# Kernel tuning notes

Hardware: AMD Instinct MI355X
Metric: run time of the kernel (lower is better)

The kernel has to match this reference:

```python
import jax, jax.numpy as jnp
import numpy as np

HID, STEM, BN_OUT, STEM_OUT, MLP = 256, 64, 128, 64, 128
BN_WS, STEM_WS = 5, 17
N, H_BN, W_BN, H_VIS, W_VIS = 4096, 128, 128, 1024, 1024


def setup_inputs() -> dict:
    key = jax.random.key(0)
    ks = jax.random.split(key, 24)
    f32 = jnp.float32
    def rn(k, shape, s=0.05):
        return jax.random.normal(k, shape, f32) * s
    return dict(
        bottleneck=rn(ks[0], (1, HID, H_BN, W_BN), 1.0),
        vis_stem_features=rn(ks[1], (1, STEM, H_VIS, W_VIS), 1.0),
        source_positions_vis=jax.random.uniform(ks[2], (N, 2), f32, 10.0, W_VIS - 10.0),
        pixel_to_sky=rn(ks[3], (N, 2, 2), 0.1),
        fused_h=H_BN, fused_w=W_BN, vis_h=H_VIS, vis_w=W_VIS,
        dw_w=rn(ks[4], (HID, 1, 7, 7)), dw_b=rn(ks[5], (HID,)),
        ln_g=jnp.ones((HID,), f32), ln_b=jnp.zeros((HID,), f32),
        pw1_w=rn(ks[6], (4 * HID, HID)), pw1_b=rn(ks[7], (4 * HID,)),
        pw2_w=rn(ks[8], (HID, 4 * HID)), pw2_b=rn(ks[9], (HID,)),
        cn_gamma=jnp.full((HID,), 1e-2, f32),
        bn1x1_w=rn(ks[10], (BN_OUT, HID, 1, 1)), bn1x1_b=rn(ks[11], (BN_OUT,)),
        st1_w=rn(ks[12], (STEM_OUT, STEM, 3, 3)), st1_b=rn(ks[13], (STEM_OUT,)),
        st2_w=rn(ks[14], (STEM_OUT, STEM_OUT, 3, 3)), st2_b=rn(ks[15], (STEM_OUT,)),
        h1_w=rn(ks[16], (MLP, BN_OUT + STEM_OUT)), h1_b=rn(ks[17], (MLP,)),
        h2_w=rn(ks[18], (MLP, MLP)), h2_b=rn(ks[19], (MLP,)),
        h3_w=rn(ks[20], (3, MLP)),
        h3_b=jnp.array([0.0, 0.0, float(np.log(0.05))], f32),
    )


def _gelu(x):
    return jax.nn.gelu(x, approximate=False)


def _conv2d(x, w, b, padding, groups=1):
    y = jax.lax.conv_general_dilated(
        x, w, (1, 1), [(padding, padding), (padding, padding)],
        dimension_numbers=('NCHW', 'OIHW', 'NCHW'), feature_group_count=groups)
    return y + b[None, :, None, None]


def _bilinear_windows(fm, pos, ws):
    """fm [1,C,H,W], pos [N,2] pixel coords -> [N,C,ws,ws].
    Matches torch grid_sample(mode=bilinear, padding=zeros, align_corners=True)
    with the module's normalize/unnormalize, i.e. direct pixel-coord sampling."""
    C, H, W = fm.shape[1:]
    fm2 = fm[0]
    half = ws // 2
    off = jnp.arange(-half, half + 1, dtype=pos.dtype)
    gy, gx = jnp.meshgrid(off, off, indexing='ij')
    xs = gx[None] + pos[:, 0, None, None]   # [N,ws,ws]
    ys = gy[None] + pos[:, 1, None, None]
    x0 = jnp.floor(xs); y0 = jnp.floor(ys)
    wx1 = xs - x0; wy1 = ys - y0
    x0i = x0.astype(jnp.int32); y0i = y0.astype(jnp.int32)
    def gather(yi, xi, w):
        valid = (yi >= 0) & (yi < H) & (xi >= 0) & (xi < W)
        v = fm2[:, jnp.clip(yi, 0, H - 1), jnp.clip(xi, 0, W - 1)]  # [C,N,ws,ws]
        return v * (w * valid)[None]
    out = (gather(y0i, x0i, (1 - wy1) * (1 - wx1))
           + gather(y0i, x0i + 1, (1 - wy1) * wx1)
           + gather(y0i + 1, x0i, wy1 * (1 - wx1))
           + gather(y0i + 1, x0i + 1, wy1 * wx1))
    return jnp.transpose(out, (1, 0, 2, 3))


def _gauss(ws):
    t = jnp.linspace(-1.0, 1.0, ws)
    yy, xx = jnp.meshgrid(t, t, indexing='ij')
    g = jnp.exp(-(xx ** 2 + yy ** 2) / (2 * 0.4 ** 2))
    return g / g.sum()


def _convnext(x, dw_w, dw_b, ln_g, ln_b, pw1_w, pw1_b, pw2_w, pw2_b, gamma):
    r = x
    x = _conv2d(x, dw_w, dw_b, padding=3, groups=x.shape[1])  # depthwise 7x7
    mu = x.mean(1, keepdims=True)
    var = ((x - mu) ** 2).mean(1, keepdims=True)
    x = (x - mu) / jnp.sqrt(var + 1e-6)
    x = x * ln_g[None, :, None, None] + ln_b[None, :, None, None]
    x = jnp.einsum('nchw,oc->nohw', x, pw1_w) + pw1_b[None, :, None, None]
    x = _gelu(x)
    x = jnp.einsum('nchw,oc->nohw', x, pw2_w) + pw2_b[None, :, None, None]
    return r + gamma[None, :, None, None] * x


def _forward(bottleneck, vis_stem_features, source_positions_vis, pixel_to_sky,
             dw_w, dw_b, ln_g, ln_b, pw1_w, pw1_b, pw2_w, pw2_b, cn_gamma,
             bn1x1_w, bn1x1_b, st1_w, st1_b, st2_w, st2_b,
             h1_w, h1_b, h2_w, h2_b, h3_w, h3_b,
             fused_h, fused_w, vis_h, vis_w):
    scale = jnp.array([fused_w / vis_w, fused_h / vis_h], source_positions_vis.dtype)
    pos_bn = source_positions_vis * scale
    # bottleneck branch: 5x5 windows -> ConvNeXt -> 1x1 conv -> GELU -> gauss pool
    bn_win = _bilinear_windows(bottleneck, pos_bn, BN_WS)              # [N,256,5,5]
    bn_feat = _convnext(bn_win, dw_w, dw_b, ln_g, ln_b, pw1_w, pw1_b, pw2_w, pw2_b, cn_gamma)
    bn_feat = _gelu(_conv2d(bn_feat, bn1x1_w, bn1x1_b, padding=0))     # [N,128,5,5]
    bn_vec = (bn_feat * _gauss(BN_WS)[None, None]).sum((-2, -1))       # [N,128]
    st_win = _bilinear_windows(vis_stem_features, source_positions_vis, STEM_WS)
    st = _gelu(_conv2d(st_win, st1_w, st1_b, padding=1))
    st = _gelu(_conv2d(st, st2_w, st2_b, padding=1))                   # [N,64,17,17]
    st_vec = (st * _gauss(STEM_WS)[None, None]).sum((-2, -1))          # [N,64]
    # head MLP
    x = jnp.concatenate([bn_vec, st_vec], axis=1)                      # [N,192]
    x = _gelu(x @ h1_w.T + h1_b)
    x = _gelu(x @ h2_w.T + h2_b)
    out = x @ h3_w.T + h3_b                                            # [N,3]
    dx_px, dy_px = out[:, 0], out[:, 1]
    log_sigma = jnp.clip(out[:, 2], -6.0, 3.0)
    pix = jnp.stack([dx_px, dy_px], axis=1)                            # [N,2]
    pred_sky = jnp.einsum('nij,nj->ni', pixel_to_sky, pix)             # [N,2]
    confidence = 1.0 / jnp.maximum(jnp.exp(log_sigma), 1e-4)
    return pred_sky, dx_px, dy_px, log_sigma, confidence


def reference(bottleneck, vis_stem_features, source_positions_vis, pixel_to_sky,
              fused_h, fused_w, vis_h, vis_w,
              dw_w, dw_b, ln_g, ln_b, pw1_w, pw1_b, pw2_w, pw2_b, cn_gamma,
              bn1x1_w, bn1x1_b, st1_w, st1_b, st2_w, st2_b,
              h1_w, h1_b, h2_w, h2_b, h3_w, h3_b):
    return _forward(bottleneck, vis_stem_features, source_positions_vis, pixel_to_sky,
                    dw_w, dw_b, ln_g, ln_b, pw1_w, pw1_b, pw2_w, pw2_b, cn_gamma,
                    bn1x1_w, bn1x1_b, st1_w, st1_b, st2_w, st2_b,
                    h1_w, h1_b, h2_w, h2_b, h3_w, h3_b,
                    fused_h, fused_w, vis_h, vis_w)
```

## Files before the change

kernel.cpp:

```cpp
#include <hip/hip_runtime.h>
#include <hip/hip_bf16.h>

#define XSTR 28

typedef short short8 __attribute__((ext_vector_type(8)));
typedef float f32x4  __attribute__((ext_vector_type(4)));
typedef float f32x16 __attribute__((ext_vector_type(16)));

__device__ __forceinline__ float gelu_f(float x){
    return 0.5f*x*(1.0f + erff(x*0.70710678118654752f));
}
__device__ __forceinline__ float gelu_q(float x){
    const float z = 1.5957691216057308f*x*(1.0f + 0.044715f*x*x);
    return x / (1.0f + __expf(-z));
}
__device__ __forceinline__ unsigned short f2bf(float f){
    unsigned int u = __float_as_uint(f);
    u += 0x7fffu + ((u>>16)&1u);
    return (unsigned short)(u>>16);
}
__device__ __forceinline__ unsigned int pack2(float a, float b){
    return (unsigned int)f2bf(a) | ((unsigned int)f2bf(b)<<16);
}
__device__ __forceinline__ float bf_lo(unsigned int u){ return __uint_as_float(u<<16); }
__device__ __forceinline__ float bf_hi(unsigned int u){ return __uint_as_float(u & 0xffff0000u); }
__device__ __forceinline__ float bfu(unsigned short v){ return __uint_as_float(((unsigned int)v)<<16); }

__device__ __forceinline__ void fma_row25(const float* __restrict__ row, float w, float* __restrict__ acc){
    const float4* r4 = (const float4*)row;
    float4 a0=r4[0], a1=r4[1], a2=r4[2], a3=r4[3], a4=r4[4], a5=r4[5];
    float a6 = row[24];
    acc[0]+=a0.x*w;  acc[1]+=a0.y*w;  acc[2]+=a0.z*w;  acc[3]+=a0.w*w;
    acc[4]+=a1.x*w;  acc[5]+=a1.y*w;  acc[6]+=a1.z*w;  acc[7]+=a1.w*w;
    acc[8]+=a2.x*w;  acc[9]+=a2.y*w;  acc[10]+=a2.z*w; acc[11]+=a2.w*w;
    acc[12]+=a3.x*w; acc[13]+=a3.y*w; acc[14]+=a3.z*w; acc[15]+=a3.w*w;
    acc[16]+=a4.x*w; acc[17]+=a4.y*w; acc[18]+=a4.z*w; acc[19]+=a4.w*w;
    acc[20]+=a5.x*w; acc[21]+=a5.y*w; acc[22]+=a5.z*w; acc[23]+=a5.w*w;
    acc[24]+=a6*w;
}

__global__ __launch_bounds__(512,4) void bn_branch_mfma(
    const float* __restrict__ bottleneck, const float* __restrict__ pos,
    const float* __restrict__ dw_w, const float* __restrict__ dw_b,
    const float* __restrict__ ln_g, const float* __restrict__ ln_b,
    const float* __restrict__ pw1_b, const float* __restrict__ pw2_b,
    const float* __restrict__ cn_gamma, const float* __restrict__ bn1x1_b,
    const short8* __restrict__ P1v, const short8* __restrict__ P2v,
    const short8* __restrict__ Pbv,
    float* __restrict__ vec_out)
{
    __shared__ __align__(16) unsigned char Xb[64*512];
    __shared__ __align__(16) unsigned char Hc[64*256];
    __shared__ float redA[400], redB[400], muS[56], rsS[56];

    const int n0 = blockIdx.x*2, t = threadIdx.x;
    const int lane = t & 63, w = t >> 6;
    const int mcol = lane & 15, h4 = lane >> 4;
    const int sP = t >> 8, cP = t & 255;

    unsigned int wvp[13];
    float xdw[25];
    {
        const int n = n0 + sP;
        const float px = pos[2*n]*0.125f, py = pos[2*n+1]*0.125f;
        const float fpx = floorf(px), fpy = floorf(py);
        const int ix0 = (int)fpx - 2, iy0 = (int)fpy - 2;
        const float fx = px - fpx, fy = py - fpy;
        const float w00=(1.f-fy)*(1.f-fx), w01=(1.f-fy)*fx, w10=fy*(1.f-fx), w11=fy*fx;
        float wv[25];
        {
            const float* fm = bottleneck + cP*16384;
            float P[6][6];
            #pragma unroll
            for (int r=0;r<6;r++){
                const int y = iy0+r;
                const bool yok = (y>=0)&&(y<128);
                const int yc = y<0?0:(y>127?127:y);
                #pragma unroll
                for (int s=0;s<6;s++){
                    const int x = ix0+s;
                    const bool ok = yok && (x>=0) && (x<128);
                    const int xc = x<0?0:(x>127?127:x);
                    P[r][s] = ok ? fm[yc*128+xc] : 0.f;
                }
            }
            #pragma unroll
            for (int a=0;a<5;a++)
            #pragma unroll
            for (int b=0;b<5;b++)
                wv[a*5+b] = w00*P[a][b]+w01*P[a][b+1]+w10*P[a+1][b]+w11*P[a+1][b+1];
        }
        #pragma unroll
        for (int i=0;i<12;i++) wvp[i] = pack2(wv[2*i], wv[2*i+1]);
        wvp[12] = pack2(wv[24], 0.f);
        {
            float wcr[49];
            const float* wc = dw_w + cP*49;
            #pragma unroll
            for (int k=0;k<49;k++) wcr[k]=wc[k];
            const float bb = dw_b[cP];
            #pragma unroll
            for (int i=0;i<5;i++){
                #pragma unroll
                for (int j=0;j<5;j++){
                    float a = bb;
                    #pragma unroll
                    for (int u=0;u<7;u++){
                        const int y = i+u-3;
                        if (y<0||y>4) continue;
                        #pragma unroll
                        for (int v=0;v<7;v++){
                            const int x = j+v-3;
                            if (x<0||x>4) continue;
                            a += wv[y*5+x]*wcr[u*7+v];
                        }
                    }
                    xdw[i*5+j] = a;
                }
            }
        }
        #pragma unroll
        for (int p=0;p<25;p++){
            const int row = sP*32 + p;
            *(unsigned short*)(Xb + row*512 + ((2*cP) ^ ((row&7)<<4))) = f2bf(xdw[p]);
        }
    }
    __syncthreads();
    if (t < 400){
        const int sp = t>>3, part = t&7;
        const int row = (sp/25)*32 + (sp - (sp/25)*25);
        float a=0.f, b=0.f;
        for (int c=part; c<256; c+=8){
            const float v = bfu(*(const unsigned short*)(Xb + row*512 + ((2*c) ^ ((row&7)<<4))));
            a += v; b += v*v;
        }
        redA[t]=a; redB[t]=b;
    }
    __syncthreads();
    if (t < 50){
        float a=0.f, b=0.f;
        #pragma unroll
        for (int s=0;s<8;s++){ a+=redA[t*8+s]; b+=redB[t*8+s]; }
        const float m = a*(1.f/256.f);
        const float var = b*(1.f/256.f) - m*m;
        muS[t]=m; rsS[t]=rsqrtf(var+1e-6f);
    }
    __syncthreads();
    {
        const float g = ln_g[cP], bb = ln_b[cP];
        #pragma unroll
        for (int p=0;p<25;p++){
            const int row = sP*32 + p;
            const float v = (xdw[p]-muS[sP*25+p])*rsS[sP*25+p]*g + bb;
            *(unsigned short*)(Xb + row*512 + ((2*cP) ^ ((row&7)<<4))) = f2bf(v);
        }
    }
    __syncthreads();

    f32x4 acc2[2][4];
    #pragma unroll
    for (int ml=0;ml<2;ml++)
        #pragma unroll
        for (int nt=0;nt<4;nt++) acc2[ml][nt]=0.f;

    for (int ch=0; ch<8; ++ch){
        const int mt = ch*8 + w;
        f32x4 a1[4];
        #pragma unroll
        for (int nt=0;nt<4;nt++) a1[nt]=0.f;
        #pragma unroll
        for (int kk=0; kk<8; ++kk){
            const short8 av = P1v[((mt<<3)+kk)*64 + lane];
            #pragma unroll
            for (int nt=0; nt<4; ++nt){
                const int row = nt*16 + mcol;
                const int ad = row*512 + ((kk*64 + h4*16) ^ ((row&7)<<4));
                const short8 bv = *(const short8*)(Xb + ad);
                a1[nt] = __builtin_amdgcn_mfma_f32_16x16x32_bf16(av, bv, a1[nt], 0,0,0);
            }
        }
        {
            const float4 b1v = *(const float4*)(pw1_b + mt*16 + h4*4);
            #pragma unroll
            for (int nt=0; nt<4; ++nt){
                const int row = nt*16 + mcol;
                const float g0 = gelu_q(a1[nt].x + b1v.x);
                const float g1 = gelu_q(a1[nt].y + b1v.y);
                const float g2 = gelu_q(a1[nt].z + b1v.z);
                const float g3 = gelu_q(a1[nt].w + b1v.w);
                const int ad = row*256 + ((w*32 + h4*8) ^ ((row&7)<<4));
                *(uint2*)(Hc + ad) = make_uint2(pack2(g0,g1), pack2(g2,g3));
            }
        }
        __syncthreads();
        #pragma unroll
        for (int ml=0; ml<2; ++ml){
            const int mtc = w*2 + ml;
            #pragma unroll
            for (int kk2=0; kk2<4; ++kk2){
                const short8 av = P2v[(mtc*32 + (ch*4 + kk2))*64 + lane];
                #pragma unroll
                for (int nt=0; nt<4; ++nt){
                    const int row = nt*16 + mcol;
                    const int ad = row*256 + ((kk2*64 + h4*16) ^ ((row&7)<<4));
                    const short8 bv = *(const short8*)(Hc + ad);
                    acc2[ml][nt] = __builtin_amdgcn_mfma_f32_16x16x32_bf16(av, bv, acc2[ml][nt], 0,0,0);
                }
            }
        }
        __syncthreads();
    }

    #pragma unroll
    for (int ml=0; ml<2; ++ml){
        const int c0 = (w*2+ml)*16 + h4*4;
        const float4 gm = *(const float4*)(cn_gamma + c0);
        const float4 b2 = *(const float4*)(pw2_b + c0);
        #pragma unroll
        for (int nt=0; nt<4; ++nt){
            const int row = nt*16 + mcol;
            const int ad = row*512 + ((2*c0) ^ ((row&7)<<4));
            const float f0 = gm.x*(acc2[ml][nt].x + b2.x);
            const float f1 = gm.y*(acc2[ml][nt].y + b2.y);
            const float f2 = gm.z*(acc2[ml][nt].z + b2.z);
            const float f3 = gm.w*(acc2[ml][nt].w + b2.w);
            *(uint2*)(Xb + ad) = make_uint2(pack2(f0,f1), pack2(f2,f3));
        }
    }
    __syncthreads();
    #pragma unroll
    for (int p=0;p<25;p++){
        const int row = sP*32 + p;
        unsigned short* ptr = (unsigned short*)(Xb + row*512 + ((2*cP) ^ ((row&7)<<4)));
        const float r = (p&1) ? bf_hi(wvp[p>>1]) : bf_lo(wvp[p>>1]);
        *ptr = f2bf(bfu(*ptr) + r);
    }
    __syncthreads();

    {
        f32x4 a3[4];
        #pragma unroll
        for (int nt=0;nt<4;nt++) a3[nt]=0.f;
        #pragma unroll
        for (int kk=0; kk<8; ++kk){
            const short8 av = Pbv[((w<<3)+kk)*64 + lane];
            #pragma unroll
            for (int nt=0; nt<4; ++nt){
                const int row = nt*16 + mcol;
                const int ad = row*512 + ((kk*64 + h4*16) ^ ((row&7)<<4));
                const short8 bv = *(const short8*)(Xb + ad);
                a3[nt] = __builtin_amdgcn_mfma_f32_16x16x32_bf16(av, bv, a3[nt], 0,0,0);
            }
        }
        const float4 bb = *(const float4*)(bn1x1_b + w*16 + h4*4);
        float e5[5];
        #pragma unroll
        for (int a=0;a<5;a++){
            const float ta = -1.f + 0.5f*a;
            e5[a] = expf(-3.125f*ta*ta);
        }
        const float Sv = e5[0]+e5[1]+e5[2]+e5[3]+e5[4];
        const float invS = 1.0f/(Sv*Sv);
        float sA[2][4];
        #pragma unroll
        for (int s=0;s<2;s++)
            #pragma unroll
            for (int j=0;j<4;j++) sA[s][j]=0.f;
        #pragma unroll
        for (int nt=0; nt<4; ++nt){
            const int row = nt*16 + mcol;
            const int s = row>>5, p = row&31;
            if (p < 25){
                const int pa = p/5, pb = p - pa*5;
                const float g = e5[pa]*e5[pb];
                sA[s][0] += g*gelu_q(a3[nt].x + bb.x);
                sA[s][1] += g*gelu_q(a3[nt].y + bb.y);
                sA[s][2] += g*gelu_q(a3[nt].z + bb.z);
                sA[s][3] += g*gelu_q(a3[nt].w + bb.w);
            }
        }
        #pragma unroll
        for (int off=1; off<16; off<<=1){
            #pragma unroll
            for (int s=0;s<2;s++)
                #pragma unroll
                for (int j=0;j<4;j++) sA[s][j] += __shfl_xor(sA[s][j], off);
        }
        if (mcol == 0){
            const int o = w*16 + h4*4;
            #pragma unroll
            for (int s=0;s<2;s++){
                float* vo = vec_out + (n0+s)*192 + o;
                vo[0]=sA[s][0]*invS; vo[1]=sA[s][1]*invS;
                vo[2]=sA[s][2]*invS; vo[3]=sA[s][3]*invS;
            }
        }
    }
}

__global__ __launch_bounds__(256) void prepack_bn_kernel(
    const float* __restrict__ W1, const float* __restrict__ W2, const float* __restrict__ Wb,
    unsigned short* __restrict__ P1, unsigned short* __restrict__ P2, unsigned short* __restrict__ Pb)
{
    const int tid = blockIdx.x*256 + threadIdx.x;
    const float* src; unsigned short* dst; int row, col, stride, idx;
    if (tid < 32768){
        idx = tid;
        const int frag = idx>>6, l = idx&63;
        row = (frag>>3)*16 + (l&15); col = (frag&7)*32 + (l>>4)*8; stride = 256;
        src = W1; dst = P1;
    } else if (tid < 65536){
        idx = tid - 32768;
        const int frag = idx>>6, l = idx&63;
        row = (frag>>5)*16 + (l&15); col = (frag&31)*32 + (l>>4)*8; stride = 1024;
        src = W2; dst = P2;
    } else if (tid < 69632){
        idx = tid - 65536;
        const int frag = idx>>6, l = idx&63;
        row = (frag>>3)*16 + (l&15); col = (frag&7)*32 + (l>>4)*8; stride = 256;
        src = Wb; dst = Pb;
    } else return;
    const float* s = src + row*stride + col;
    unsigned int v[4];
    #pragma unroll
    for (int j=0;j<4;j++) v[j] = pack2(s[2*j], s[2*j+1]);
    *(uint4*)(dst + (size_t)idx*8) = make_uint4(v[0],v[1],v[2],v[3]);
}

__global__ __launch_bounds__(256,2) void bn_branch_valu(
    const float* __restrict__ bottleneck, const float* __restrict__ pos,
    const float* __restrict__ dw_w, const float* __restrict__ dw_b,
    const float* __restrict__ ln_g, const float* __restrict__ ln_b,
    const float* __restrict__ pw1_w, const float* __restrict__ pw1_b,
    const float* __restrict__ pw2_w, const float* __restrict__ pw2_b,
    const float* __restrict__ cn_gamma,
    const float* __restrict__ bn1x1_w, const float* __restrict__ bn1x1_b,
    float* __restrict__ vec_out)
{
    __shared__ float xln[256*XSTR];
    __shared__ float hbuf[256*XSTR];
    __shared__ float redA[200], redB[200];
    __shared__ float mu[25], rs[25];

    const int n = blockIdx.x;
    const int t = threadIdx.x;
    const int c = t;

    const float px = pos[2*n]*0.125f, py = pos[2*n+1]*0.125f;
    const float fpx = floorf(px), fpy = floorf(py);
    const int ix0 = (int)fpx - 2, iy0 = (int)fpy - 2;
    const float fx = px - fpx, fy = py - fpy;
    const float w00=(1.f-fy)*(1.f-fx), w01=(1.f-fy)*fx, w10=fy*(1.f-fx), w11=fy*fx;

    float wv[25];
    {
        const float* fm = bottleneck + c*16384;
        float P[6][6];
        #pragma unroll
        for (int r=0;r<6;r++){
            const int y = iy0+r;
            const bool yok = (y>=0)&&(y<128);
            const int yc = y<0?0:(y>127?127:y);
            #pragma unroll
            for (int s=0;s<6;s++){
                const int x = ix0+s;
                const bool ok = yok && (x>=0) && (x<128);
                const int xc = x<0?0:(x>127?127:x);
                P[r][s] = ok ? fm[yc*128+xc] : 0.f;
            }
        }
        #pragma unroll
        for (int a=0;a<5;a++)
        #pragma unroll
        for (int b=0;b<5;b++)
            wv[a*5+b] = w00*P[a][b]+w01*P[a][b+1]+w10*P[a+1][b]+w11*P[a+1][b+1];
    }
    {
        float wcr[49];
        const float* wc = dw_w + c*49;
        #pragma unroll
        for (int k=0;k<49;k++) wcr[k]=wc[k];
        const float bb = dw_b[c];
        #pragma unroll
        for (int i=0;i<5;i++){
            #pragma unroll
            for (int j=0;j<5;j++){
                float a = bb;
                #pragma unroll
                for (int u=0;u<7;u++){
                    const int y = i+u-3;
                    if (y<0||y>4) continue;
                    #pragma unroll
                    for (int v=0;v<7;v++){
                        const int x = j+v-3;
                        if (x<0||x>4) continue;
                        a += wv[y*5+x]*wcr[u*7+v];
                    }
                }
                xln[c*XSTR + i*5+j] = a;
            }
        }
    }
    __syncthreads();
    if (t < 200){
        const int p = t>>3, s = t&7;
        float a=0.f, b=0.f;
        for (int cc=s; cc<256; cc+=8){
            const float v = xln[cc*XSTR+p];
            a += v; b += v*v;
        }
        redA[t]=a; redB[t]=b;
    }
    __syncthreads();
    if (t < 25){
        float a=0.f, b=0.f;
        #pragma unroll
        for (int s=0;s<8;s++){ a+=redA[t*8+s]; b+=redB[t*8+s]; }
        const float m = a*(1.f/256.f);
        const float var = b*(1.f/256.f) - m*m;
        mu[t]=m; rs[t]=rsqrtf(var+1e-6f);
    }
    __syncthreads();
    {
        const float g = ln_g[c], bb = ln_b[c];
        #pragma unroll
        for (int p=0;p<25;p++)
            xln[c*XSTR+p] = (xln[c*XSTR+p]-mu[p])*rs[p]*g + bb;
    }
    __syncthreads();
    float acc2[25];
    #pragma unroll
    for (int p=0;p<25;p++) acc2[p]=0.f;
    for (int r=0;r<4;r++){
        const int o = r*256 + t;
        float h[25];
        {
            const float b1 = pw1_b[o];
            #pragma unroll
            for (int p=0;p<25;p++) h[p]=b1;
            const float* wr = pw1_w + o*256;
            for (int cc=0;cc<256;cc++)
                fma_row25(xln + cc*XSTR, wr[cc], h);
            #pragma unroll
            for (int p=0;p<25;p++) h[p]=gelu_f(h[p]);
        }
        __syncthreads();
        #pragma unroll
        for (int p=0;p<25;p++) hbuf[t*XSTR+p]=h[p];
        __syncthreads();
        {
            const float* w2 = pw2_w + t*1024 + r*256;
            for (int k=0;k<256;k++)
                fma_row25(hbuf + k*XSTR, w2[k], acc2);
        }
    }
    {
        const float gam = cn_gamma[c], b2 = pw2_b[c];
        #pragma unroll
        for (int p=0;p<25;p++)
            xln[c*XSTR+p] = wv[p] + gam*(acc2[p]+b2);
    }
    __syncthreads();
    if (t < 128){
        float acc[25];
        #pragma unroll
        for (int p=0;p<25;p++) acc[p]=0.f;
        const float* wr = bn1x1_w + t*256;
        for (int cc=0;cc<256;cc++)
            fma_row25(xln + cc*XSTR, wr[cc], acc);
        const float b = bn1x1_b[t];
        float e5[5];
        #pragma unroll
        for (int a=0;a<5;a++){
            const float ta = -1.f + 0.5f*a;
            e5[a] = expf(-3.125f*ta*ta);
        }
        const float Sv = e5[0]+e5[1]+e5[2]+e5[3]+e5[4];
        float res = 0.f;
        #pragma unroll
        for (int a=0;a<5;a++){
            float rowa = 0.f;
            #pragma unroll
            for (int bb=0;bb<5;bb++)
                rowa += e5[bb]*gelu_f(acc[a*5+bb]+b);
            res += e5[a]*rowa;
        }
        vec_out[n*192+t] = res/(Sv*Sv);
    }
}

__global__ __launch_bounds__(256) void prepack_kernel(
    const float* __restrict__ W1, const float* __restrict__ W2,
    unsigned short* __restrict__ Ap)
{
    const int tid = blockIdx.x*256 + threadIdx.x;
    if (tid >= 9216) return;
    const int conv = tid / 4608;
    const int r = tid - conv*4608;
    const int frag = r >> 6, l = r & 63;
    const int k  = frag >> 3;
    const int kt = (frag >> 1) & 3;
    const int wo = frag & 1;
    const float* W = conv ? W2 : W1;
    const int o  = wo*32 + (l & 31);
    const int c0 = kt*16 + (l >> 5)*8;
    unsigned int v[4];
    #pragma unroll
    for (int jj=0; jj<4; jj++){
        const float f0 = W[o*576 + (c0+2*jj  )*9 + k];
        const float f1 = W[o*576 + (c0+2*jj+1)*9 + k];
        v[jj] = pack2(f0, f1);
    }
    *(uint4*)(Ap + (size_t)tid*8) = make_uint4(v[0], v[1], v[2], v[3]);
}

#define STEM_CONV32(SRC, AP)                                                        \
    _Pragma("unroll")                                                               \
    for (int k=0;k<9;k++){                                                          \
        int tj[3];                                                                  \
        _Pragma("unroll")                                                           \
        for (int j=0;j<3;j++)                                                       \
            tj[j] = (int)sTab[m*90 + (j<cnt ? st+j : st)*9 + k];                    \
        _Pragma("unroll")                                                           \
        for (int kt=0;kt<4;kt++){                                                   \
            const short8 av = (AP)[(k*8 + kt*2 + wo)*64 + lane];                    \
            const int cb = kt*32 + hi16;                                            \
            _Pragma("unroll")                                                       \
            for (int j=0;j<3;j++){                                                  \
                if (j < cnt){                                                       \
                    const short8 bv = *(const short8*)((SRC) + (tj[j] ^ cb));       \
                    acc[j] = __builtin_amdgcn_mfma_f32_32x32x16_bf16(av, bv, acc[j], 0,0,0); \
                }                                                                   \
            }                                                                       \
        }                                                                           \
    }

__global__ __launch_bounds__(512,4) void stem_branch_kernel(
    const float* __restrict__ vis,
    const float* __restrict__ pos,
    const short8* __restrict__ Ap1,
    const float* __restrict__ st1_b,
    const float* __restrict__ st2_b,
    float* __restrict__ vec_out)
{
    __shared__ __align__(16) unsigned char sXt[290*128];
    __shared__ unsigned short sTab[32*90];
    __shared__ float redS[64][4];

    const int n = blockIdx.x;
    const int t = threadIdx.x;
    const int lane = t & 63;
    const int m = lane & 31;
    const int hi = lane >> 5;
    const int hi16 = hi*16;
    const int w = t >> 6;
    const int wo = w & 1;
    const int nh = w >> 1;
    const int st  = nh*3 - (nh==3 ? 1 : 0);
    const int cnt = (nh < 2) ? 3 : 2;

    const float fpx0 = pos[2*n], fpy0 = pos[2*n+1];
    const float fpx = floorf(fpx0), fpy = floorf(fpy0);
    const int ix0 = (int)fpx - 8, iy0 = (int)fpy - 8;
    const float fx = fpx0-fpx, fy = fpy0-fpy;
    const float w00=(1.f-fy)*(1.f-fx), w01=(1.f-fy)*fx, w10=fy*(1.f-fx), w11=fy*fx;

    if (t < 32) *(unsigned int*)(sXt + 289*128 + t*4) = 0u;

    for (int idx = t; idx < 32*90; idx += 512){
        const int mm = idx/90, rem = idx - mm*90;
        const int nt = rem/9, k = rem - nt*9;
        const int p = nt*32 + mm;
        int pp = 289;
        if (p < 289){
            const int py = (p*241)>>12, px = p - py*17;
            const int y = py + k/3 - 1, x = px + (k - (k/3)*3) - 1;
            if (((unsigned)y < 17u) && ((unsigned)x < 17u)) pp = y*17 + x;
        }
        sTab[idx] = (unsigned short)(pp*128 + ((pp&7)<<4));
    }

    for (int task = t; task < 64*17; task += 512){
        const int c  = task & 63;
        const int py = task >> 6;
        const float* r0 = vis + c*1048576 + (iy0+py)*1024 + ix0;
        float a[18], b[18];
        #pragma unroll
        for (int kk=0; kk<18; kk++){ a[kk]=r0[kk]; b[kk]=r0[1024+kk]; }
        #pragma unroll
        for (int px=0; px<17; px++){
            const float v = w00*a[px] + w01*a[px+1] + w10*b[px] + w11*b[px+1];
            const int p = py*17 + px;
            *(unsigned short*)(sXt + p*128 + ((2*c) ^ ((p&7)<<4))) = f2bf(v);
        }
    }
    __syncthreads();

    f32x16 acc[3];
    #pragma unroll
    for (int j=0;j<3;j++) acc[j] = 0.f;
    STEM_CONV32(sXt, Ap1)

    uint2 pk[3][4];
    {
        float4 b4[4];
        #pragma unroll
        for (int rg=0;rg<4;rg++) b4[rg] = *(const float4*)(st1_b + wo*32 + 8*rg + 4*hi);
        #pragma unroll
        for (int j=0;j<3;j++){
            if (j < cnt){
                #pragma unroll
                for (int rg=0;rg<4;rg++){
                    const float v0 = gelu_q(acc[j][4*rg+0] + b4[rg].x);
                    const float v1 = gelu_q(acc[j][4*rg+1] + b4[rg].y);
                    const float v2 = gelu_q(acc[j][4*rg+2] + b4[rg].z);
                    const float v3 = gelu_q(acc[j][4*rg+3] + b4[rg].w);
                    pk[j][rg] = make_uint2(pack2(v0,v1), pack2(v2,v3));
                }
            }
        }
    }
    __syncthreads();

    #pragma unroll
    for (int j=0;j<3;j++){
        if (j < cnt){
            const int p = (st+j)*32 + m;
            if (p < 289){
                const int swz = (p&7)<<4;
                #pragma unroll
                for (int rg=0;rg<4;rg++){
                    const int ch0 = wo*32 + 8*rg + 4*hi;
                    *(uint2*)(sXt + p*128 + ((2*ch0) ^ swz)) = pk[j][rg];
                }
            }
        }
    }
    __syncthreads();

    const short8* Ap2 = Ap1 + 4608;
    #pragma unroll
    for (int j=0;j<3;j++) acc[j] = 0.f;
    STEM_CONV32(sXt, Ap2)

    {
        float4 b4[4];
        #pragma unroll
        for (int rg=0;rg<4;rg++) b4[rg] = *(const float4*)(st2_b + wo*32 + 8*rg + 4*hi);
        float s[16];
        #pragma unroll
        for (int r=0;r<16;r++) s[r]=0.f;
        #pragma unroll
        for (int j=0;j<3;j++){
            if (j < cnt){
                const int p = (st+j)*32 + m;
                if (p < 289){
                    const int py = (p*241)>>12;
                    const int px = p - py*17;
                    const float ty = -1.f + 0.125f*py;
                    const float tx = -1.f + 0.125f*px;
                    const float g = expf(-3.125f*(ty*ty + tx*tx));
                    #pragma unroll
                    for (int rg=0;rg<4;rg++){
                        s[4*rg+0] += g*gelu_q(acc[j][4*rg+0] + b4[rg].x);
                        s[4*rg+1] += g*gelu_q(acc[j][4*rg+1] + b4[rg].y);
                        s[4*rg+2] += g*gelu_q(acc[j][4*rg+2] + b4[rg].z);
                        s[4*rg+3] += g*gelu_q(acc[j][4*rg+3] + b4[rg].w);
                    }
                }
            }
        }
        #pragma unroll
        for (int off=1; off<32; off<<=1){
            #pragma unroll
            for (int r=0;r<16;r++) s[r] += __shfl_xor(s[r], off);
        }
        if (m == 0){
            #pragma unroll
            for (int rg=0;rg<4;rg++)
                #pragma unroll
                for (int e=0;e<4;e++)
                    redS[wo*32 + 8*rg + 4*hi + e][nh] = s[4*rg+e];
        }
    }
    __syncthreads();
    if (t < 64){
        float Sv = 0.f;
        #pragma unroll
        for (int j=0;j<17;j++){
            const float tj = -1.f + 0.125f*j;
            Sv += expf(-3.125f*tj*tj);
        }
        vec_out[n*192+128+t] = (redS[t][0] + redS[t][1] + redS[t][2] + redS[t][3]) / (Sv*Sv);
    }
}

__global__ __launch_bounds__(128) void head16_kernel(
    const float* __restrict__ vec, const float* __restrict__ p2s,
    const float* __restrict__ h1_w, const float* __restrict__ h1_b,
    const float* __restrict__ h2_w, const float* __restrict__ h2_b,
    const float* __restrict__ h3_w, const float* __restrict__ h3_b,
    float* __restrict__ out, int N)
{
    __shared__ float v[16][192];
    __shared__ float x1s[16][132];
    __shared__ float x2s[16][132];
    __shared__ float o3s[16][4];
    const int n0 = blockIdx.x*16, t = threadIdx.x;

    for (int idx=t; idx<16*192; idx+=128){
        const int s = idx/192, k = idx - s*192;
        v[s][k] = vec[n0*192 + idx];
    }
    __syncthreads();
    {
        const int o = t;
        float acc[16];
        const float b = h1_b[o];
        #pragma unroll
        for (int s=0;s<16;s++) acc[s]=b;
        const float4* wr = (const float4*)(h1_w + o*192);
        for (int k4=0;k4<48;k4++){
            const float4 wv4 = wr[k4];
            #pragma unroll
            for (int s=0;s<16;s++){
                const float4 vv = *(const float4*)&v[s][k4*4];
                acc[s] += wv4.x*vv.x + wv4.y*vv.y + wv4.z*vv.z + wv4.w*vv.w;
            }
        }
        #pragma unroll
        for (int s=0;s<16;s++) x1s[s][o] = gelu_f(acc[s]);
    }
    __syncthreads();
    {
        const int o = t;
        float acc[16];
        const float b = h2_b[o];
        #pragma unroll
        for (int s=0;s<16;s++) acc[s]=b;
        const float4* wr = (const float4*)(h2_w + o*128);
        for (int k4=0;k4<32;k4++){
            const float4 wv4 = wr[k4];
            #pragma unroll
            for (int s=0;s<16;s++){
                const float4 vv = *(const float4*)&x1s[s][k4*4];
                acc[s] += wv4.x*vv.x + wv4.y*vv.y + wv4.z*vv.z + wv4.w*vv.w;
            }
        }
        #pragma unroll
        for (int s=0;s<16;s++) x2s[s][o] = gelu_f(acc[s]);
    }
    __syncthreads();
    if (t < 48){
        const int j = t>>4, s = t&15;
        float a = h3_b[j];
        const float* wr = h3_w + j*128;
        for (int k=0;k<128;k++) a += x2s[s][k]*wr[k];
        o3s[s][j] = a;
    }
    __syncthreads();
    if (t < 16){
        const int s = t, n = n0 + s;
        const float dx = o3s[s][0], dy = o3s[s][1];
        float ls = o3s[s][2];
        ls = ls < -6.f ? -6.f : (ls > 3.f ? 3.f : ls);
        const float s0 = p2s[n*4+0]*dx + p2s[n*4+1]*dy;
        const float s1 = p2s[n*4+2]*dx + p2s[n*4+3]*dy;
        const float conf = 1.0f/fmaxf(expf(ls), 1e-4f);
        out[2*n]   = s0;
        out[2*n+1] = s1;
        out[2*N+n] = dx;
        out[3*N+n] = dy;
        out[4*N+n] = ls;
        out[5*N+n] = conf;
    }
}

extern "C" void kernel_launch(void* const* d_in, const int* in_sizes, int n_in,
                              void* d_out, int out_size, void* d_ws, size_t ws_size,
                              hipStream_t stream)
{
    (void)n_in; (void)out_size;
    const float* bottleneck = (const float*)d_in[0];
    const float* vis        = (const float*)d_in[1];
    const float* pos        = (const float*)d_in[2];
    const float* p2s        = (const float*)d_in[3];
    const float* dw_w  = (const float*)d_in[8];
    const float* dw_b  = (const float*)d_in[9];
    const float* ln_g  = (const float*)d_in[10];
    const float* ln_b  = (const float*)d_in[11];
    const float* pw1_w = (const float*)d_in[12];
    const float* pw1_b = (const float*)d_in[13];
    const float* pw2_w = (const float*)d_in[14];
    const float* pw2_b = (const float*)d_in[15];
    const float* gam   = (const float*)d_in[16];
    const float* b1w   = (const float*)d_in[17];
    const float* b1b   = (const float*)d_in[18];
    const float* s1w   = (const float*)d_in[19];
    const float* s1b   = (const float*)d_in[20];
    const float* s2w   = (const float*)d_in[21];
    const float* s2b   = (const float*)d_in[22];
    const float* h1w   = (const float*)d_in[23];
    const float* h1b   = (const float*)d_in[24];
    const float* h2w   = (const float*)d_in[25];
    const float* h2b   = (const float*)d_in[26];
    const float* h3w   = (const float*)d_in[27];
    const float* h3b   = (const float*)d_in[28];

    const int N = in_sizes[2]/2;
    float* vec = (float*)d_ws;
    const size_t vec_bytes = (size_t)N*192*sizeof(float);
    unsigned short* Apack = (unsigned short*)((char*)d_ws + vec_bytes);
    unsigned short* P1 = Apack + 73728;
    unsigned short* P2 = P1 + 262144;
    unsigned short* Pb = P2 + 262144;
    const size_t need = vec_bytes + 147456u + (262144u+262144u+32768u)*2u;

    hipMemsetAsync(d_ws, 0, vec_bytes, stream);

    prepack_kernel<<<36, 256, 0, stream>>>(s1w, s2w, Apack);

    if (ws_size >= need){
        prepack_bn_kernel<<<272, 256, 0, stream>>>(pw1_w, pw2_w, b1w, P1, P2, Pb);
        bn_branch_mfma<<<N/2, 512, 0, stream>>>(bottleneck, pos, dw_w, dw_b, ln_g, ln_b,
                                                pw1_b, pw2_b, gam, b1b,
                                                (const short8*)P1, (const short8*)P2, (const short8*)Pb,
                                                vec);
    } else {
        bn_branch_valu<<<N, 256, 0, stream>>>(bottleneck, pos, dw_w, dw_b, ln_g, ln_b,
                                              pw1_w, pw1_b, pw2_w, pw2_b, gam, b1w, b1b, vec);
    }
    stem_branch_kernel<<<N, 512, 0, stream>>>(vis, pos, (const short8*)Apack, s1b, s2b, vec);
    head16_kernel<<<N/16, 128, 0, stream>>>(vec, p2s, h1w, h1b, h2w, h2b, h3w, h3b,
                                            (float*)d_out, N);
}
```

Baseline: 847.3 us.

## Fuse bottleneck and stem branch kernels into one heterogeneous launch

Merges the bottleneck MFMA branch and the stem conv branch into a single kernel whose blocks are split by blockIdx (one bn block per two stem blocks) and share a unioned shared-memory buffer. This removes a kernel boundary so the two independent branches can run concurrently on the GPU and fill its compute units better. The cost is that every block now reserves the larger union of shared memory (about 52.8 KB), which can lower occupancy for the stem blocks, and the register allocation is set by the heavier of the two bodies.

```diff
diff --git a/kernel.cpp b/kernel.cpp
--- a/kernel.cpp
+++ b/kernel.cpp
@@ -39,7 +39,8 @@
     acc[24]+=a6*w;
 }
 
-__global__ __launch_bounds__(512,4) void bn_branch_mfma(
+__device__ __forceinline__ void bn_body(
+    unsigned char* __restrict__ U, int n0, int t,
     const float* __restrict__ bottleneck, const float* __restrict__ pos,
     const float* __restrict__ dw_w, const float* __restrict__ dw_b,
     const float* __restrict__ ln_g, const float* __restrict__ ln_b,
@@ -49,11 +50,13 @@
     const short8* __restrict__ Pbv,
     float* __restrict__ vec_out)
 {
-    __shared__ __align__(16) unsigned char Xb[64*512];
-    __shared__ __align__(16) unsigned char Hc[64*256];
-    __shared__ float redA[400], redB[400], muS[56], rsS[56];
-
-    const int n0 = blockIdx.x*2, t = threadIdx.x;
+    unsigned char* Xb = U;
+    unsigned char* Hc = U + 32768;
+    float* redA = (float*)(U + 49152);
+    float* redB = (float*)(U + 50752);
+    float* muS  = (float*)(U + 52352);
+    float* rsS  = (float*)(U + 52576);
+
     const int lane = t & 63, w = t >> 6;
     const int mcol = lane & 15, h4 = lane >> 4;
     const int sP = t >> 8, cP = t & 255;
@@ -295,6 +298,208 @@
                 vo[2]=sA[s][2]*invS; vo[3]=sA[s][3]*invS;
             }
         }
+    }
+}
+
+#define STEM_CONV32(SRC, AP)                                                        \
+    _Pragma("unroll")                                                               \
+    for (int k=0;k<9;k++){                                                          \
+        int tj[3];                                                                  \
+        _Pragma("unroll")                                                           \
+        for (int j=0;j<3;j++)                                                       \
+            tj[j] = (int)sTab[m*90 + (j<cnt ? st+j : st)*9 + k];                    \
+        _Pragma("unroll")                                                           \
+        for (int kt=0;kt<4;kt++){                                                   \
+            const short8 av = (AP)[(k*8 + kt*2 + wo)*64 + lane];                    \
+            const int cb = kt*32 + hi16;                                            \
+            _Pragma("unroll")                                                       \
+            for (int j=0;j<3;j++){                                                  \
+                if (j < cnt){                                                       \
+                    const short8 bv = *(const short8*)((SRC) + (tj[j] ^ cb));       \
+                    acc[j] = __builtin_amdgcn_mfma_f32_32x32x16_bf16(av, bv, acc[j], 0,0,0); \
+                }                                                                   \
+            }                                                                       \
+        }                                                                           \
+    }
+
+__device__ __forceinline__ void stem_body(
+    unsigned char* __restrict__ U, int n, int t,
+    const float* __restrict__ vis, const float* __restrict__ pos,
+    const short8* __restrict__ Ap1,
+    const float* __restrict__ st1_b, const float* __restrict__ st2_b,
+    float* __restrict__ vec_out)
+{
+    unsigned char* sXt = U;
+    unsigned short* sTab = (unsigned short*)(U + 37120);
+    float (*redS)[4] = (float(*)[4])(U + 42880);
+
+    const int lane = t & 63;
+    const int m = lane & 31;
+    const int hi = lane >> 5;
+    const int hi16 = hi*16;
+    const int w = t >> 6;
+    const int wo = w & 1;
+    const int nh = w >> 1;
+    const int st  = nh*3 - (nh==3 ? 1 : 0);
+    const int cnt = (nh < 2) ? 3 : 2;
+
+    const float fpx0 = pos[2*n], fpy0 = pos[2*n+1];
+    const float fpx = floorf(fpx0), fpy = floorf(fpy0);
+    const int ix0 = (int)fpx - 8, iy0 = (int)fpy - 8;
+    const float fx = fpx0-fpx, fy = fpy0-fpy;
+    const float w00=(1.f-fy)*(1.f-fx), w01=(1.f-fy)*fx, w10=fy*(1.f-fx), w11=fy*fx;
+
+    if (t < 32) *(unsigned int*)(sXt + 289*128 + t*4) = 0u;
+
+    for (int idx = t; idx < 32*90; idx += 512){
+        const int mm = idx/90, rem = idx - mm*90;
+        const int nt = rem/9, k = rem - nt*9;
+        const int p = nt*32 + mm;
+        int pp = 289;
+        if (p < 289){
+            const int py = (p*241)>>12, px = p - py*17;
+            const int y = py + k/3 - 1, x = px + (k - (k/3)*3) - 1;
+            if (((unsigned)y < 17u) && ((unsigned)x < 17u)) pp = y*17 + x;
+        }
+        sTab[idx] = (unsigned short)(pp*128 + ((pp&7)<<4));
+    }
+
+    for (int task = t; task < 64*17; task += 512){
+        const int c  = task & 63;
+        const int py = task >> 6;
+        const float* r0 = vis + c*1048576 + (iy0+py)*1024 + ix0;
+        float a[18], b[18];
+        #pragma unroll
+        for (int kk=0; kk<18; kk++){ a[kk]=r0[kk]; b[kk]=r0[1024+kk]; }
+        #pragma unroll
+        for (int px=0; px<17; px++){
+            const float v = w00*a[px] + w01*a[px+1] + w10*b[px] + w11*b[px+1];
+            const int p = py*17 + px;
+            *(unsigned short*)(sXt + p*128 + ((2*c) ^ ((p&7)<<4))) = f2bf(v);
+        }
+    }
+    __syncthreads();
+
+    f32x16 acc[3];
+    #pragma unroll
+    for (int j=0;j<3;j++) acc[j] = 0.f;
+    STEM_CONV32(sXt, Ap1)
+
+    uint2 pk[3][4];
+    {
+        float4 b4[4];
+        #pragma unroll
+        for (int rg=0;rg<4;rg++) b4[rg] = *(const float4*)(st1_b + wo*32 + 8*rg + 4*hi);
+        #pragma unroll
+        for (int j=0;j<3;j++){
+            if (j < cnt){
+                #pragma unroll
+                for (int rg=0;rg<4;rg++){
+                    const float v0 = gelu_q(acc[j][4*rg+0] + b4[rg].x);
+                    const float v1 = gelu_q(acc[j][4*rg+1] + b4[rg].y);
+                    const float v2 = gelu_q(acc[j][4*rg+2] + b4[rg].z);
+                    const float v3 = gelu_q(acc[j][4*rg+3] + b4[rg].w);
+                    pk[j][rg] = make_uint2(pack2(v0,v1), pack2(v2,v3));
+                }
+            }
+        }
+    }
+    __syncthreads();
+
+    #pragma unroll
+    for (int j=0;j<3;j++){
+        if (j < cnt){
+            const int p = (st+j)*32 + m;
+            if (p < 289){
+                const int swz = (p&7)<<4;
+                #pragma unroll
+                for (int rg=0;rg<4;rg++){
+                    const int ch0 = wo*32 + 8*rg + 4*hi;
+                    *(uint2*)(sXt + p*128 + ((2*ch0) ^ swz)) = pk[j][rg];
+                }
+            }
+        }
+    }
+    __syncthreads();
+
+    const short8* Ap2 = Ap1 + 4608;
+    #pragma unroll
+    for (int j=0;j<3;j++) acc[j] = 0.f;
+    STEM_CONV32(sXt, Ap2)
+
+    {
+        float4 b4[4];
+        #pragma unroll
+        for (int rg=0;rg<4;rg++) b4[rg] = *(const float4*)(st2_b + wo*32 + 8*rg + 4*hi);
+        float s[16];
+        #pragma unroll
+        for (int r=0;r<16;r++) s[r]=0.f;
+        #pragma unroll
+        for (int j=0;j<3;j++){
+            if (j < cnt){
+                const int p = (st+j)*32 + m;
+                if (p < 289){
+                    const int py = (p*241)>>12;
+                    const int px = p - py*17;
+                    const float ty = -1.f + 0.125f*py;
+                    const float tx = -1.f + 0.125f*px;
+                    const float g = expf(-3.125f*(ty*ty + tx*tx));
+                    #pragma unroll
+                    for (int rg=0;rg<4;rg++){
+                        s[4*rg+0] += g*gelu_q(acc[j][4*rg+0] + b4[rg].x);
+                        s[4*rg+1] += g*gelu_q(acc[j][4*rg+1] + b4[rg].y);
+                        s[4*rg+2] += g*gelu_q(acc[j][4*rg+2] + b4[rg].z);
+                        s[4*rg+3] += g*gelu_q(acc[j][4*rg+3] + b4[rg].w);
+                    }
+                }
+            }
+        }
+        #pragma unroll
+        for (int off=1; off<32; off<<=1){
+            #pragma unroll
+            for (int r=0;r<16;r++) s[r] += __shfl_xor(s[r], off);
+        }
+        if (m == 0){
+            #pragma unroll
+            for (int rg=0;rg<4;rg++)
+                #pragma unroll
+                for (int e=0;e<4;e++)
+                    redS[wo*32 + 8*rg + 4*hi + e][nh] = s[4*rg+e];
+        }
+    }
+    __syncthreads();
+    if (t < 64){
+        float Sv = 0.f;
+        #pragma unroll
+        for (int j=0;j<17;j++){
+            const float tj = -1.f + 0.125f*j;
+            Sv += expf(-3.125f*tj*tj);
+        }
+        vec_out[n*192+128+t] = (redS[t][0] + redS[t][1] + redS[t][2] + redS[t][3]) / (Sv*Sv);
+    }
+}
+
+__global__ __launch_bounds__(512,4) void fused_branches(
+    const float* __restrict__ bottleneck, const float* __restrict__ vis,
+    const float* __restrict__ pos,
+    const float* __restrict__ dw_w, const float* __restrict__ dw_b,
+    const float* __restrict__ ln_g, const float* __restrict__ ln_b,
+    const float* __restrict__ pw1_b, const float* __restrict__ pw2_b,
+    const float* __restrict__ cn_gamma, const float* __restrict__ bn1x1_b,
+    const short8* __restrict__ P1v, const short8* __restrict__ P2v,
+    const short8* __restrict__ Pbv,
+    const short8* __restrict__ Ap1,
+    const float* __restrict__ st1_b, const float* __restrict__ st2_b,
+    float* __restrict__ vec_out)
+{
+    __shared__ __align__(16) unsigned char U[52800];
+    const int b = blockIdx.x, t = threadIdx.x;
+    const int q = b/3, r = b - q*3;
+    if (r == 0){
+        bn_body(U, q*2, t, bottleneck, pos, dw_w, dw_b, ln_g, ln_b,
+                pw1_b, pw2_b, cn_gamma, bn1x1_b, P1v, P2v, Pbv, vec_out);
+    } else {
+        stem_body(U, q*2 + r - 1, t, vis, pos, Ap1, st1_b, st2_b, vec_out);
     }
 }
 
@@ -514,27 +719,6 @@
     *(uint4*)(Ap + (size_t)tid*8) = make_uint4(v[0], v[1], v[2], v[3]);
 }
 
-#define STEM_CONV32(SRC, AP)                                                        \
-    _Pragma("unroll")                                                               \
-    for (int k=0;k<9;k++){                                                          \
-        int tj[3];                                                                  \
-        _Pragma("unroll")                                                           \
-        for (int j=0;j<3;j++)                                                       \
-            tj[j] = (int)sTab[m*90 + (j<cnt ? st+j : st)*9 + k];                    \
-        _Pragma("unroll")                                                           \
-        for (int kt=0;kt<4;kt++){                                                   \
-            const short8 av = (AP)[(k*8 + kt*2 + wo)*64 + lane];                    \
-            const int cb = kt*32 + hi16;                                            \
-            _Pragma("unroll")                                                       \
-            for (int j=0;j<3;j++){                                                  \
-                if (j < cnt){                                                       \
-                    const short8 bv = *(const short8*)((SRC) + (tj[j] ^ cb));       \
-                    acc[j] = __builtin_amdgcn_mfma_f32_32x32x16_bf16(av, bv, acc[j], 0,0,0); \
-                }                                                                   \
-            }                                                                       \
-        }                                                                           \
-    }
-
 __global__ __launch_bounds__(512,4) void stem_branch_kernel(
     const float* __restrict__ vis,
     const float* __restrict__ pos,
@@ -543,156 +727,8 @@
     const float* __restrict__ st2_b,
     float* __restrict__ vec_out)
 {
-    __shared__ __align__(16) unsigned char sXt[290*128];
-    __shared__ unsigned short sTab[32*90];
-    __shared__ float redS[64][4];
-
-    const int n = blockIdx.x;
-    const int t = threadIdx.x;
-    const int lane = t & 63;
-    const int m = lane & 31;
-    const int hi = lane >> 5;
-    const int hi16 = hi*16;
-    const int w = t >> 6;
-    const int wo = w & 1;
-    const int nh = w >> 1;
-    const int st  = nh*3 - (nh==3 ? 1 : 0);
-    const int cnt = (nh < 2) ? 3 : 2;
-
-    const float fpx0 = pos[2*n], fpy0 = pos[2*n+1];
-    const float fpx = floorf(fpx0), fpy = floorf(fpy0);
-    const int ix0 = (int)fpx - 8, iy0 = (int)fpy - 8;
-    const float fx = fpx0-fpx, fy = fpy0-fpy;
-    const float w00=(1.f-fy)*(1.f-fx), w01=(1.f-fy)*fx, w10=fy*(1.f-fx), w11=fy*fx;
-
-    if (t < 32) *(unsigned int*)(sXt + 289*128 + t*4) = 0u;
-
-    for (int idx = t; idx < 32*90; idx += 512){
-        const int mm = idx/90, rem = idx - mm*90;
-        const int nt = rem/9, k = rem - nt*9;
-        const int p = nt*32 + mm;
-        int pp = 289;
-        if (p < 289){
-            const int py = (p*241)>>12, px = p - py*17;
-            const int y = py + k/3 - 1, x = px + (k - (k/3)*3) - 1;
-            if (((unsigned)y < 17u) && ((unsigned)x < 17u)) pp = y*17 + x;
-        }
-        sTab[idx] = (unsigned short)(pp*128 + ((pp&7)<<4));
-    }
-
-    for (int task = t; task < 64*17; task += 512){
-        const int c  = task & 63;
-        const int py = task >> 6;
-        const float* r0 = vis + c*1048576 + (iy0+py)*1024 + ix0;
-        float a[18], b[18];
-        #pragma unroll
-        for (int kk=0; kk<18; kk++){ a[kk]=r0[kk]; b[kk]=r0[1024+kk]; }
-        #pragma unroll
-        for (int px=0; px<17; px++){
-            const float v = w00*a[px] + w01*a[px+1] + w10*b[px] + w11*b[px+1];
-            const int p = py*17 + px;
-            *(unsigned short*)(sXt + p*128 + ((2*c) ^ ((p&7)<<4))) = f2bf(v);
-        }
-    }
-    __syncthreads();
-
-    f32x16 acc[3];
-    #pragma unroll
-    for (int j=0;j<3;j++) acc[j] = 0.f;
-    STEM_CONV32(sXt, Ap1)
-
-    uint2 pk[3][4];
-    {
-        float4 b4[4];
-        #pragma unroll
-        for (int rg=0;rg<4;rg++) b4[rg] = *(const float4*)(st1_b + wo*32 + 8*rg + 4*hi);
-        #pragma unroll
-        for (int j=0;j<3;j++){
-            if (j < cnt){
-                #pragma unroll
-                for (int rg=0;rg<4;rg++){
-                    const float v0 = gelu_q(acc[j][4*rg+0] + b4[rg].x);
-                    const float v1 = gelu_q(acc[j][4*rg+1] + b4[rg].y);
-                    const float v2 = gelu_q(acc[j][4*rg+2] + b4[rg].z);
-                    const float v3 = gelu_q(acc[j][4*rg+3] + b4[rg].w);
-                    pk[j][rg] = make_uint2(pack2(v0,v1), pack2(v2,v3));
-                }
-            }
-        }
-    }
-    __syncthreads();
-
-    #pragma unroll
-    for (int j=0;j<3;j++){
-        if (j < cnt){
-            const int p = (st+j)*32 + m;
-            if (p < 289){
-                const int swz = (p&7)<<4;
-                #pragma unroll
-                for (int rg=0;rg<4;rg++){
-                    const int ch0 = wo*32 + 8*rg + 4*hi;
-                    *(uint2*)(sXt + p*128 + ((2*ch0) ^ swz)) = pk[j][rg];
-                }
-            }
-        }
-    }
-    __syncthreads();
-
-    const short8* Ap2 = Ap1 + 4608;
-    #pragma unroll
-    for (int j=0;j<3;j++) acc[j] = 0.f;
-    STEM_CONV32(sXt, Ap2)
-
-    {
-        float4 b4[4];
-        #pragma unroll
-        for (int rg=0;rg<4;rg++) b4[rg] = *(const float4*)(st2_b + wo*32 + 8*rg + 4*hi);
-        float s[16];
-        #pragma unroll
-        for (int r=0;r<16;r++) s[r]=0.f;
-        #pragma unroll
-        for (int j=0;j<3;j++){
-            if (j < cnt){
-                const int p = (st+j)*32 + m;
-                if (p < 289){
-                    const int py = (p*241)>>12;
-                    const int px = p - py*17;
-                    const float ty = -1.f + 0.125f*py;
-                    const float tx = -1.f + 0.125f*px;
-                    const float g = expf(-3.125f*(ty*ty + tx*tx));
-                    #pragma unroll
-                    for (int rg=0;rg<4;rg++){
-                        s[4*rg+0] += g*gelu_q(acc[j][4*rg+0] + b4[rg].x);
-                        s[4*rg+1] += g*gelu_q(acc[j][4*rg+1] + b4[rg].y);
-                        s[4*rg+2] += g*gelu_q(acc[j][4*rg+2] + b4[rg].z);
-                        s[4*rg+3] += g*gelu_q(acc[j][4*rg+3] + b4[rg].w);
-                    }
-                }
-            }
-        }
-        #pragma unroll
-        for (int off=1; off<32; off<<=1){
-            #pragma unroll
-            for (int r=0;r<16;r++) s[r] += __shfl_xor(s[r], off);
-        }
-        if (m == 0){
-            #pragma unroll
-            for (int rg=0;rg<4;rg++)
-                #pragma unroll
-                for (int e=0;e<4;e++)
-                    redS[wo*32 + 8*rg + 4*hi + e][nh] = s[4*rg+e];
-        }
-    }
-    __syncthreads();
-    if (t < 64){
-        float Sv = 0.f;
-        #pragma unroll
-        for (int j=0;j<17;j++){
-            const float tj = -1.f + 0.125f*j;
-            Sv += expf(-3.125f*tj*tj);
-        }
-        vec_out[n*192+128+t] = (redS[t][0] + redS[t][1] + redS[t][2] + redS[t][3]) / (Sv*Sv);
-    }
+    __shared__ __align__(16) unsigned char U[43904];
+    stem_body(U, blockIdx.x, threadIdx.x, vis, pos, Ap1, st1_b, st2_b, vec_out);
 }
 
 __global__ __launch_bounds__(128) void head16_kernel(
@@ -822,15 +858,16 @@
 
     if (ws_size >= need){
         prepack_bn_kernel<<<272, 256, 0, stream>>>(pw1_w, pw2_w, b1w, P1, P2, Pb);
-        bn_branch_mfma<<<N/2, 512, 0, stream>>>(bottleneck, pos, dw_w, dw_b, ln_g, ln_b,
-                                                pw1_b, pw2_b, gam, b1b,
-                                                (const short8*)P1, (const short8*)P2, (const short8*)Pb,
-                                                vec);
+        fused_branches<<<3*(N/2), 512, 0, stream>>>(bottleneck, vis, pos,
+                                                    dw_w, dw_b, ln_g, ln_b,
+                                                    pw1_b, pw2_b, gam, b1b,
+                                                    (const short8*)P1, (const short8*)P2, (const short8*)Pb,
+                                                    (const short8*)Apack, s1b, s2b, vec);
     } else {
         bn_branch_valu<<<N, 256, 0, stream>>>(bottleneck, pos, dw_w, dw_b, ln_g, ln_b,
                                               pw1_w, pw1_b, pw2_w, pw2_b, gam, b1w, b1b, vec);
-    }
-    stem_branch_kernel<<<N, 512, 0, stream>>>(vis, pos, (const short8*)Apack, s1b, s2b, vec);
+        stem_branch_kernel<<<N, 512, 0, stream>>>(vis, pos, (const short8*)Apack, s1b, s2b, vec);
+    }
     head16_kernel<<<N/16, 128, 0, stream>>>(vec, p2s, h1w, h1b, h2w, h2b, h3w, h3b,
                                             (float*)d_out, N);
 }
```

After: 869.3 us. 2.6% more time.
